# Optimization experiments

Hardware: AMD Instinct MI355X
Metric: run time of the kernel (lower is better)

The kernel has to match this reference:

```python
import jax, jax.numpy as jnp
import numpy as np

N_NODES = 50000
N_EDGES = 800000
D_FEAT = 128
D_EMB = 128


def setup_inputs() -> dict:
    key = jax.random.key(0)
    k1, k2, k3, k4, k5 = jax.random.split(key, 5)
    feature = jax.random.normal(k1, (N_NODES, D_FEAT), dtype=jnp.float32)
    edge_src = jax.random.randint(k2, (N_EDGES,), 0, N_NODES, dtype=jnp.int32)
    edge_dst = jax.random.randint(k3, (N_EDGES,), 0, N_NODES, dtype=jnp.int32)
    edge_w = jax.random.uniform(k4, (N_EDGES,), dtype=jnp.float32)
    # reset_parameters: uniform(-stdv, stdv), stdv = 1/sqrt(embedding_size)
    stdv = 1.0 / np.sqrt(D_EMB)
    weight = jax.random.uniform(k5, (D_FEAT, D_EMB), dtype=jnp.float32,
                                minval=-stdv, maxval=stdv)
    return {"feature": feature, "edge_src": edge_src, "edge_dst": edge_dst,
            "edge_w": edge_w, "weight": weight}


def reference(feature, edge_src, edge_dst, edge_w, weight):
    # spmm(adj, feature): out[dst] += w * feature[src]
    msgs = edge_w[:, None] * feature[edge_src]          # [E, D_FEAT]
    agg = jax.ops.segment_sum(msgs, edge_dst, num_segments=feature.shape[0])
    # residual blend then dense projection
    blended = 0.5 * agg + 0.5 * feature                  # [N, D_FEAT]
    return blended @ weight                              # [N, D_EMB]
```

## Files before the change

### kernel.cpp

```cpp
#include <hip/hip_runtime.h>

#define N_NODES 50000
#define N_EDGES 800000
#define D 128
#define NBUCK 196
#define CAP 4800
#define CHUNK 4096
#define PA_BLKS ((N_EDGES + CHUNK - 1) / CHUNK)
#define FB_BLKS 12500
#define WT_BLKS 64

typedef __attribute__((ext_vector_type(8))) short short8;
typedef __attribute__((ext_vector_type(4))) float f32x4;

__device__ __forceinline__ unsigned short f2bf(float f) {
    unsigned u = __float_as_uint(f);
    u += 0x7fff + ((u >> 16) & 1);
    return (unsigned short)(u >> 16);
}

__global__ __launch_bounds__(256) void prep_passA(
    const float2* __restrict__ feat2, unsigned* __restrict__ fb,
    const float* __restrict__ W, unsigned short* __restrict__ Wt,
    const int* __restrict__ esrc, const int* __restrict__ edst,
    const float* __restrict__ ew, int* __restrict__ gcur,
    uint2* __restrict__ tmp) {
    __shared__ int lh[NBUCK], lbase[NBUCK], lcur[NBUCK];
    int blk = blockIdx.x, t = threadIdx.x;

    if (blk >= PA_BLKS) {
        int b2 = blk - PA_BLKS;
        if (b2 < FB_BLKS) {
            int i = b2 * 256 + t;
            float2 f = feat2[i];
            fb[i] = (unsigned)f2bf(f.x) | ((unsigned)f2bf(f.y) << 16);
        } else {
            int idx = (b2 - FB_BLKS) * 256 + t;
            int n = idx >> 7, k = idx & 127;
            Wt[idx] = f2bf(W[k * 128 + n]);
        }
        return;
    }

    for (int i = t; i < NBUCK; i += 256) lh[i] = 0;
    __syncthreads();
    int e0 = blk * CHUNK;
    unsigned key[16];
    float wv[16];
#pragma unroll
    for (int j = 0; j < 16; ++j) {
        int e = e0 + j * 256 + t;
        if (e < N_EDGES) {
            int src = esrc[e], dd = edst[e];
            key[j] = (unsigned)src | ((unsigned)(dd & 255) << 16) |
                     ((unsigned)(dd >> 8) << 24);
            wv[j] = ew[e];
            atomicAdd(&lh[dd >> 8], 1);
        } else key[j] = 0xff000000u;
    }
    __syncthreads();
    for (int i = t; i < NBUCK; i += 256) {
        lbase[i] = atomicAdd(&gcur[i], lh[i]);
        lcur[i] = 0;
    }
    __syncthreads();
#pragma unroll
    for (int j = 0; j < 16; ++j) {
        int b = key[j] >> 24;
        if (b < NBUCK) {
            int r = atomicAdd(&lcur[b], 1);
            tmp[(size_t)b * CAP + lbase[b] + r] =
                make_uint2(key[j] & 0x00ffffffu, __float_as_uint(wv[j]));
        }
    }
}

__global__ __launch_bounds__(256) void passB(const int* __restrict__ gcur,
                                             const uint2* __restrict__ tmp,
                                             int* __restrict__ offsets,
                                             uint2* __restrict__ sw) {
    __shared__ int gb[NBUCK];
    __shared__ int hist[256], ps[256];
    __shared__ int sbase;
    int b = blockIdx.x, t = threadIdx.x;
    for (int i = t; i < NBUCK; i += 256) gb[i] = gcur[i];
    hist[t] = 0;
    __syncthreads();
    if (t == 0) {
        int run = 0;
        for (int i = 0; i < b; ++i) run += gb[i];
        sbase = run;
    }
    __syncthreads();
    int base = sbase, cnt = gb[b];
    const uint2* seg = tmp + (size_t)b * CAP;

    for (int i = t; i < cnt; i += 256) atomicAdd(&hist[seg[i].x >> 16], 1);
    __syncthreads();
    int h = hist[t];
    ps[t] = h;
    __syncthreads();
    for (int off = 1; off < 256; off <<= 1) {
        int x = (t >= off) ? ps[t - off] : 0;
        __syncthreads();
        ps[t] += x;
        __syncthreads();
    }
    int o = base + ps[t] - h;
    int node = b * 256 + t;
    if (node < N_NODES) offsets[node] = o;
    if (b == NBUCK - 1 && t == 0) offsets[N_NODES] = N_EDGES;
    __syncthreads();
    hist[t] = o;
    __syncthreads();
    for (int i = t; i < cnt; i += 256) {
        uint2 u = seg[i];
        int pos = atomicAdd(&hist[u.x >> 16], 1);
        sw[pos] = make_uint2(u.x & 0xffffu, u.y);
    }
}

__global__ __launch_bounds__(256) void agg_gemm(const int* __restrict__ offsets,
                                                const uint2* __restrict__ sw,
                                                const unsigned* __restrict__ fb,
                                                const unsigned short* __restrict__ Wt,
                                                float* __restrict__ out) {
    __shared__ unsigned Arows[16][68];
    int wave = threadIdx.x >> 6;
    int lane = threadIdx.x & 63;
    int row0 = blockIdx.x * 16;

#pragma unroll 1
    for (int i = 0; i < 4; ++i) {
        int n = row0 + wave * 4 + i;
        n = __builtin_amdgcn_readfirstlane(n);
        int b = offsets[n], e2 = offsets[n + 1];
        unsigned us = fb[(size_t)n * 64 + lane];
        float ax = 0.f, ay = 0.f;
        int e = b;
        for (; e + 16 <= e2; e += 16) {
            uint2 p[16];
            unsigned u[16];
#pragma unroll
            for (int j = 0; j < 16; ++j) p[j] = sw[e + j];
#pragma unroll
            for (int j = 0; j < 16; ++j) u[j] = fb[(size_t)p[j].x * 64 + lane];
#pragma unroll
            for (int j = 0; j < 16; ++j) {
                float w = __uint_as_float(p[j].y);
                ax += w * __uint_as_float(u[j] << 16);
                ay += w * __uint_as_float(u[j] & 0xffff0000u);
            }
        }
        if (e + 8 <= e2) {
            uint2 p[8];
            unsigned u[8];
#pragma unroll
            for (int j = 0; j < 8; ++j) p[j] = sw[e + j];
#pragma unroll
            for (int j = 0; j < 8; ++j) u[j] = fb[(size_t)p[j].x * 64 + lane];
#pragma unroll
            for (int j = 0; j < 8; ++j) {
                float w = __uint_as_float(p[j].y);
                ax += w * __uint_as_float(u[j] << 16);
                ay += w * __uint_as_float(u[j] & 0xffff0000u);
            }
            e += 8;
        }
        for (; e < e2; ++e) {
            uint2 p = sw[e];
            unsigned u = fb[(size_t)p.x * 64 + lane];
            float w = __uint_as_float(p.y);
            ax += w * __uint_as_float(u << 16);
            ay += w * __uint_as_float(u & 0xffff0000u);
        }
        float rx = 0.5f * (ax + __uint_as_float(us << 16));
        float ry = 0.5f * (ay + __uint_as_float(us & 0xffff0000u));
        Arows[wave * 4 + i][lane] = (unsigned)f2bf(rx) | ((unsigned)f2bf(ry) << 16);
    }
    __syncthreads();

    int quad = lane >> 4;
    int col  = lane & 15;
    short8 a[4];
#pragma unroll
    for (int kk = 0; kk < 4; ++kk)
        a[kk] = *reinterpret_cast<const short8*>(&Arows[col][kk * 16 + quad * 4]);

#pragma unroll
    for (int ii = 0; ii < 2; ++ii) {
        int n0 = wave * 2 + ii;
        const short8* bp = reinterpret_cast<const short8*>(Wt) + ((n0 * 16 + col) * 16 + quad);
        f32x4 acc = {0.f, 0.f, 0.f, 0.f};
        acc = __builtin_amdgcn_mfma_f32_16x16x32_bf16(a[0], bp[0],  acc, 0, 0, 0);
        acc = __builtin_amdgcn_mfma_f32_16x16x32_bf16(a[1], bp[4],  acc, 0, 0, 0);
        acc = __builtin_amdgcn_mfma_f32_16x16x32_bf16(a[2], bp[8],  acc, 0, 0, 0);
        acc = __builtin_amdgcn_mfma_f32_16x16x32_bf16(a[3], bp[12], acc, 0, 0, 0);
#pragma unroll
        for (int rr = 0; rr < 4; ++rr)
            out[(size_t)(row0 + quad * 4 + rr) * D + n0 * 16 + col] = acc[rr];
    }
}

extern "C" void kernel_launch(void* const* d_in, const int* in_sizes, int n_in,
                              void* d_out, int out_size, void* d_ws, size_t ws_size,
                              hipStream_t stream) {
    const float* feat = (const float*)d_in[0];
    const int*   esrc = (const int*)d_in[1];
    const int*   edst = (const int*)d_in[2];
    const float* ew   = (const float*)d_in[3];
    const float* W    = (const float*)d_in[4];
    float*       out  = (float*)d_out;

    char* ws = (char*)d_ws;
    uint2*          sw      = (uint2*)(ws + 0);
    unsigned*       fb      = (unsigned*)(ws + 6400000);
    int*            offsets = (int*)(ws + 19200000);
    unsigned short* Wt      = (unsigned short*)(ws + 19400064);
    int*            gcur    = (int*)(ws + 19432832);
    uint2* tmp = (uint2*)d_out;

    hipMemsetAsync(gcur, 0, NBUCK * sizeof(int), stream);
    prep_passA<<<PA_BLKS + FB_BLKS + WT_BLKS, 256, 0, stream>>>(
        (const float2*)feat, fb, W, Wt, esrc, edst, ew, gcur, tmp);
    passB<<<NBUCK, 256, 0, stream>>>(gcur, tmp, offsets, sw);
    agg_gemm<<<N_NODES / 16, 256, 0, stream>>>(offsets, sw, fb, Wt, out);
}
```

Measured before the change: 150.5 us.

## Software-pipeline edge index loads and use masked tail in aggregation

The aggregation loop now prefetches the next 16 edge records while gathering features for the current batch. The separate 8-edge and scalar tails are replaced by one masked 16-wide tail that clamps indices and zeroes weights. passB replaces the serial prefix over bucket counts with a parallel block scan, and agg_gemm gets a minimum-occupancy launch bound. This adds register pressure and issues redundant loads for short rows in exchange for better latency hiding.

```diff
diff --git a/kernel.cpp b/kernel.cpp
--- a/kernel.cpp
+++ b/kernel.cpp
@@ -18,6 +18,8 @@
     u += 0x7fff + ((u >> 16) & 1);
     return (unsigned short)(u >> 16);
 }
+__device__ __forceinline__ float lo16f(unsigned u) { return __uint_as_float(u << 16); }
+__device__ __forceinline__ float hi16f(unsigned u) { return __uint_as_float(u & 0xffff0000u); }
 
 __global__ __launch_bounds__(256) void prep_passA(
     const float2* __restrict__ feat2, unsigned* __restrict__ fb,
@@ -79,20 +81,23 @@
                                              const uint2* __restrict__ tmp,
                                              int* __restrict__ offsets,
                                              uint2* __restrict__ sw) {
-    __shared__ int gb[NBUCK];
     __shared__ int hist[256], ps[256];
-    __shared__ int sbase;
+    __shared__ int sbase, scnt;
     int b = blockIdx.x, t = threadIdx.x;
-    for (int i = t; i < NBUCK; i += 256) gb[i] = gcur[i];
+
+    int gv = (t < NBUCK) ? gcur[t] : 0;
+    ps[t] = gv;
+    __syncthreads();
+    for (int off = 1; off < 256; off <<= 1) {
+        int x = (t >= off) ? ps[t - off] : 0;
+        __syncthreads();
+        ps[t] += x;
+        __syncthreads();
+    }
+    if (t == b) { sbase = ps[t] - gv; scnt = gv; }
     hist[t] = 0;
     __syncthreads();
-    if (t == 0) {
-        int run = 0;
-        for (int i = 0; i < b; ++i) run += gb[i];
-        sbase = run;
-    }
-    __syncthreads();
-    int base = sbase, cnt = gb[b];
+    int base = sbase, cnt = scnt;
     const uint2* seg = tmp + (size_t)b * CAP;
 
     for (int i = t; i < cnt; i += 256) atomicAdd(&hist[seg[i].x >> 16], 1);
@@ -120,11 +125,11 @@
     }
 }
 
-__global__ __launch_bounds__(256) void agg_gemm(const int* __restrict__ offsets,
-                                                const uint2* __restrict__ sw,
-                                                const unsigned* __restrict__ fb,
-                                                const unsigned short* __restrict__ Wt,
-                                                float* __restrict__ out) {
+__global__ __launch_bounds__(256, 2) void agg_gemm(const int* __restrict__ offsets,
+                                                   const uint2* __restrict__ sw,
+                                                   const unsigned* __restrict__ fb,
+                                                   const unsigned short* __restrict__ Wt,
+                                                   float* __restrict__ out) {
     __shared__ unsigned Arows[16][68];
     int wave = threadIdx.x >> 6;
     int lane = threadIdx.x & 63;
@@ -132,50 +137,59 @@
 
 #pragma unroll 1
     for (int i = 0; i < 4; ++i) {
-        int n = row0 + wave * 4 + i;
-        n = __builtin_amdgcn_readfirstlane(n);
+        int n = __builtin_amdgcn_readfirstlane(row0 + wave * 4 + i);
         int b = offsets[n], e2 = offsets[n + 1];
         unsigned us = fb[(size_t)n * 64 + lane];
         float ax = 0.f, ay = 0.f;
         int e = b;
-        for (; e + 16 <= e2; e += 16) {
-            uint2 p[16];
+        int nfull = (e2 - b) >> 4;
+
+        uint2 p[16];
+        {
+            int rem = e2 - e;
+#pragma unroll
+            for (int j = 0; j < 16; ++j) {
+                int idx = (j < rem) ? j : (rem > 0 ? rem - 1 : 0);
+                p[j] = sw[e + idx];
+            }
+        }
+#pragma unroll 1
+        for (int t = 0; t < nfull; ++t) {
             unsigned u[16];
 #pragma unroll
-            for (int j = 0; j < 16; ++j) p[j] = sw[e + j];
-#pragma unroll
             for (int j = 0; j < 16; ++j) u[j] = fb[(size_t)p[j].x * 64 + lane];
+            int en = e + 16;
+            int rem = e2 - en;
+            uint2 pn[16];
+#pragma unroll
+            for (int j = 0; j < 16; ++j) {
+                int idx = (j < rem) ? j : (rem > 0 ? rem - 1 : 0);
+                pn[j] = sw[en + idx];
+            }
 #pragma unroll
             for (int j = 0; j < 16; ++j) {
                 float w = __uint_as_float(p[j].y);
-                ax += w * __uint_as_float(u[j] << 16);
-                ay += w * __uint_as_float(u[j] & 0xffff0000u);
-            }
-        }
-        if (e + 8 <= e2) {
-            uint2 p[8];
-            unsigned u[8];
-#pragma unroll
-            for (int j = 0; j < 8; ++j) p[j] = sw[e + j];
-#pragma unroll
-            for (int j = 0; j < 8; ++j) u[j] = fb[(size_t)p[j].x * 64 + lane];
-#pragma unroll
-            for (int j = 0; j < 8; ++j) {
-                float w = __uint_as_float(p[j].y);
-                ax += w * __uint_as_float(u[j] << 16);
-                ay += w * __uint_as_float(u[j] & 0xffff0000u);
-            }
-            e += 8;
-        }
-        for (; e < e2; ++e) {
-            uint2 p = sw[e];
-            unsigned u = fb[(size_t)p.x * 64 + lane];
-            float w = __uint_as_float(p.y);
-            ax += w * __uint_as_float(u << 16);
-            ay += w * __uint_as_float(u & 0xffff0000u);
-        }
-        float rx = 0.5f * (ax + __uint_as_float(us << 16));
-        float ry = 0.5f * (ay + __uint_as_float(us & 0xffff0000u));
+                ax += w * lo16f(u[j]);
+                ay += w * hi16f(u[j]);
+            }
+#pragma unroll
+            for (int j = 0; j < 16; ++j) p[j] = pn[j];
+            e = en;
+        }
+        int rem = e2 - e;
+        if (rem > 0) {
+            unsigned u[16];
+#pragma unroll
+            for (int j = 0; j < 16; ++j) u[j] = fb[(size_t)p[j].x * 64 + lane];
+#pragma unroll
+            for (int j = 0; j < 16; ++j) {
+                float w = (j < rem) ? __uint_as_float(p[j].y) : 0.f;
+                ax += w * lo16f(u[j]);
+                ay += w * hi16f(u[j]);
+            }
+        }
+        float rx = 0.5f * (ax + lo16f(us));
+        float ry = 0.5f * (ay + hi16f(us));
         Arows[wave * 4 + i][lane] = (unsigned)f2bf(rx) | ((unsigned)f2bf(ry) << 16);
     }
     __syncthreads();
```

Measured after the change: 149.9 us. Within noise of the previous version (-0.4%).
